# Optimization experiments

Measured on AMD Instinct MI355X. Metric: run time of the kernel, lower is better.

## Reference

```python
import jax, jax.numpy as jnp
import numpy as np

N_NODES = 50000
N_EDGES = 800000
D_IN = 256
D_OUT = 256
BN_EPS = 1e-5


def setup_inputs() -> dict:
    key = jax.random.key(0)
    k1, k2, k3 = jax.random.split(key, 3)
    x = jax.random.normal(k1, (N_NODES, D_IN), dtype=jnp.float32)
    edge_index = jax.random.randint(k2, (2, N_EDGES), 0, N_NODES, dtype=jnp.int64)
    # GCNConv linear weight [out, in] (glorot-ish scale), separate bias
    W = jax.random.normal(k3, (D_OUT, D_IN), dtype=jnp.float32) * (1.0 / np.sqrt(D_IN))
    bias = jnp.zeros((D_OUT,), dtype=jnp.float32)
    gamma = jnp.ones((D_OUT,), dtype=jnp.float32)
    beta = jnp.zeros((D_OUT,), dtype=jnp.float32)
    return {"x": x, "edge_index": edge_index, "W": W, "bias": bias, "gamma": gamma, "beta": beta}


def reference(x, edge_index, W, bias, gamma, beta):
    N = x.shape[0]
    self_loops = jnp.arange(N, dtype=edge_index.dtype)
    row = jnp.concatenate([edge_index[0], self_loops])  # source nodes
    col = jnp.concatenate([edge_index[1], self_loops])  # target nodes

    # linear transform first (PyG GCNConv order): [N, D_out]
    h = x @ W.T

    # symmetric degree normalization with self-loops
    deg = jax.ops.segment_sum(jnp.ones_like(col, dtype=h.dtype), col, num_segments=N)
    dinv = jnp.where(deg > 0, jax.lax.rsqrt(deg), 0.0)
    norm = dinv[row] * dinv[col]  # [E+N]

    # gather -> scale -> scatter-add
    msg = h[row] * norm[:, None]                         # [E+N, D_out]
    agg = jax.ops.segment_sum(msg, col, num_segments=N)  # [N, D_out]
    agg = agg + bias

    # BatchNorm (training mode: batch stats over nodes, biased var)
    mean = jnp.mean(agg, axis=0)
    var = jnp.mean((agg - mean) ** 2, axis=0)
    y = gamma * (agg - mean) * jax.lax.rsqrt(var + BN_EPS) + beta
    return jax.nn.relu(y)
```

## Files before the change

### kernel.cpp

```cpp
#include <hip/hip_runtime.h>
#include <cstdio>

#define NN 50000
#define NE 800000
#define DD 256
#define CAP 32
#define WS_NEED 113080000UL

__attribute__((constructor)) static void r25_on_load(void) {
    fprintf(stderr, "R25SO_LOADED\n");
    fflush(stderr);
}

__device__ float b2f(unsigned short u) {
    union { unsigned int i; float f; } c;
    c.i = ((unsigned int)u) << 16;
    return c.f;
}
__device__ float clampf(float v) { return fminf(fmaxf(v, -65504.f), 65504.f); }
__device__ float rdF(const void* p, long long idx, int ff) {
    if (ff) return clampf(b2f(((const unsigned short*)p)[idx]));
    return clampf(((const float*)p)[idx]);
}
__device__ unsigned short f2b_rne(float f) {
    union { float f; unsigned int u; } c;
    c.f = f;
    unsigned int r = (c.u + 0x7FFFu + ((c.u >> 16) & 1u)) >> 16;
    return (unsigned short)r;
}

typedef __attribute__((ext_vector_type(8))) short bf16x8;
typedef __attribute__((ext_vector_type(4))) float f32x4;
typedef __attribute__((ext_vector_type(4))) _Float16 f16x4;
typedef __attribute__((ext_vector_type(8))) _Float16 f16x8;

__device__ int detect_ff(const unsigned short* xr) {
    __shared__ int dacc;
    if (threadIdx.x == 0) dacc = 0;
    __syncthreads();
    int g = 0;
    for (int j = 0; j < 4; j++) {
        unsigned short u = xr[(threadIdx.x * 4 + j) * 2];
        int e = (u >> 7) & 0xFF;
        if (u == 0 || u == 0x8000 || (e >= 100 && e <= 140)) g++;
    }
    atomicAdd(&dacc, g);
    __syncthreads();
    return dacc >= 922;
}

__global__ void k_setup(int* cnt, int* misc, const unsigned short* xr,
                        const int* ei, int* flags, const void* W, const void* bias,
                        const void* gamma, const void* beta, unsigned short* Wb,
                        float* pf) {
    int b = blockIdx.x;
    int t = threadIdx.x;
    if (b < 196) {
        int i = b * 256 + t;
        if (i < NN) cnt[i] = 0;
        if (i < 16) misc[i] = 0;
        return;
    }
    if (b == 196) {
        __shared__ int acc2;
        if (t == 0) acc2 = 0;
        int ff = detect_ff(xr);
        if (ei[2 * t + 1] != 0) atomicAdd(&acc2, 1);
        __syncthreads();
        if (t == 0) {
            flags[0] = ff;
            flags[1] = (acc2 == 0) ? 1 : 0;
        }
        pf[t] = rdF(bias, t, ff);
        pf[DD + t] = rdF(gamma, t, ff);
        pf[2 * DD + t] = rdF(beta, t, ff);
        return;
    }
    int ff = detect_ff(xr);
    int i = (b - 197) * 256 + t;
    Wb[i] = f2b_rne(rdF(W, i, ff));
}

__global__ void k_fill1(const int* raw, const int* flags, int* cnt, int* csrc,
                        int* ovf, int* novf) {
    int e = blockIdx.x * 256 + threadIdx.x;
    if (e >= NE) return;
    int f = flags[1];
    int r = f ? raw[2 * e] : raw[e];
    int c = f ? raw[2 * (NE + e)] : raw[NE + e];
    if ((unsigned int)c < NN && (unsigned int)r < NN) {
        int slot = atomicAdd(&cnt[c], 1);
        if (slot < CAP) {
            csrc[c * CAP + slot] = r;
        } else {
            int o = atomicAdd(novf, 1);
            ovf[2 * o] = c;
            ovf[2 * o + 1] = r;
        }
    }
}

__global__ void k_dinv(const int* cnt, float* dinv) {
    int i = blockIdx.x * 256 + threadIdx.x;
    if (i < NN) dinv[i] = rsqrtf((float)(cnt[i] + 1));
}

#define WP 264
__global__ __launch_bounds__(1024) void k_gemm(const void* x, const int* flags,
                                               const unsigned short* Wb,
                                               const float* dinv, _Float16* h) {
    __shared__ unsigned short wlds[256 * WP];
    int t = threadIdx.x;

#pragma unroll
    for (int i = 0; i < 8; i++) {
        int c = t + i * 1024;
        int row = c >> 5;
        int off = (c & 31) * 8;
        bf16x8 v = *(const bf16x8*)(Wb + row * DD + off);
        *(bf16x8*)(&wlds[row * WP + off]) = v;
    }
    __syncthreads();

    int wave = t >> 6;
    int lane = t & 63;
    int rw = blockIdx.x * 16 + wave;
    if (rw >= 3125) return;
    int r0 = rw * 16;
    int l15 = lane & 15;
    int kq = lane >> 4;

    bf16x8 a[8];
    int ff = flags[0];
    if (ff) {
        const unsigned short* p =
            (const unsigned short*)x + (unsigned long long)(r0 + l15) * DD + kq * 8;
#pragma unroll
        for (int k = 0; k < 8; k++)
            a[k] = *(const bf16x8*)(p + k * 32);
    } else {
        const float* p = (const float*)x + (unsigned long long)(r0 + l15) * DD + kq * 8;
#pragma unroll
        for (int k = 0; k < 8; k++) {
#pragma unroll
            for (int j = 0; j < 8; j++)
                a[k][j] = (short)f2b_rne(p[k * 32 + j]);
        }
    }

    float dv[4];
#pragma unroll
    for (int j = 0; j < 4; j++) dv[j] = dinv[r0 + kq * 4 + j];

#pragma unroll
    for (int ct = 0; ct < 16; ct++) {
        f32x4 acc = {0.f, 0.f, 0.f, 0.f};
#pragma unroll
        for (int k = 0; k < 8; k++) {
            bf16x8 b = *(const bf16x8*)(&wlds[(ct * 16 + l15) * WP + kq * 8 + k * 32]);
            acc = __builtin_amdgcn_mfma_f32_16x16x32_bf16(a[k], b, acc, 0, 0, 0);
        }
        _Float16* op = h + (unsigned long long)(r0 + kq * 4) * DD + ct * 16 + l15;
#pragma unroll
        for (int j = 0; j < 4; j++)
            op[(unsigned long long)j * DD] = (_Float16)(acc[j] * dv[j]);
    }
}

__global__ __launch_bounds__(256) void g_agg(const _Float16* h, const float* dinv,
                                             const int* cnt, const int* csrc,
                                             const int* ovf, const int* novf,
                                             const float* pf, _Float16* agg) {
    int lane = threadIdx.x & 63;
    int n = blockIdx.x * 4 + (threadIdx.x >> 6);
    int f0 = lane * 4;
    int cn = __builtin_amdgcn_readfirstlane(cnt[n]);
    int m = (cn < CAP) ? cn : CAP;
    float dn = dinv[n];
    f16x4 hv = *(const f16x4*)(h + (unsigned long long)n * DD + f0);
    float a0 = (float)hv[0];
    float a1 = (float)hv[1];
    float a2 = (float)hv[2];
    float a3 = (float)hv[3];
    const int* ip = csrc + n * CAP;
    int k = 0;
    for (; k + 8 <= m; k += 8) {
        int i0 = ip[k + 0], i1 = ip[k + 1], i2 = ip[k + 2], i3 = ip[k + 3];
        int i4 = ip[k + 4], i5 = ip[k + 5], i6 = ip[k + 6], i7 = ip[k + 7];
        f16x4 v0 = *(const f16x4*)(h + (unsigned long long)i0 * DD + f0);
        f16x4 v1 = *(const f16x4*)(h + (unsigned long long)i1 * DD + f0);
        f16x4 v2 = *(const f16x4*)(h + (unsigned long long)i2 * DD + f0);
        f16x4 v3 = *(const f16x4*)(h + (unsigned long long)i3 * DD + f0);
        f16x4 v4 = *(const f16x4*)(h + (unsigned long long)i4 * DD + f0);
        f16x4 v5 = *(const f16x4*)(h + (unsigned long long)i5 * DD + f0);
        f16x4 v6 = *(const f16x4*)(h + (unsigned long long)i6 * DD + f0);
        f16x4 v7 = *(const f16x4*)(h + (unsigned long long)i7 * DD + f0);
        a0 += (((float)v0[0] + (float)v1[0]) + ((float)v2[0] + (float)v3[0])) +
              (((float)v4[0] + (float)v5[0]) + ((float)v6[0] + (float)v7[0]));
        a1 += (((float)v0[1] + (float)v1[1]) + ((float)v2[1] + (float)v3[1])) +
              (((float)v4[1] + (float)v5[1]) + ((float)v6[1] + (float)v7[1]));
        a2 += (((float)v0[2] + (float)v1[2]) + ((float)v2[2] + (float)v3[2])) +
              (((float)v4[2] + (float)v5[2]) + ((float)v6[2] + (float)v7[2]));
        a3 += (((float)v0[3] + (float)v1[3]) + ((float)v2[3] + (float)v3[3])) +
              (((float)v4[3] + (float)v5[3]) + ((float)v6[3] + (float)v7[3]));
    }
    for (; k + 4 <= m; k += 4) {
        int i0 = ip[k + 0], i1 = ip[k + 1], i2 = ip[k + 2], i3 = ip[k + 3];
        f16x4 v0 = *(const f16x4*)(h + (unsigned long long)i0 * DD + f0);
        f16x4 v1 = *(const f16x4*)(h + (unsigned long long)i1 * DD + f0);
        f16x4 v2 = *(const f16x4*)(h + (unsigned long long)i2 * DD + f0);
        f16x4 v3 = *(const f16x4*)(h + (unsigned long long)i3 * DD + f0);
        a0 += ((float)v0[0] + (float)v1[0]) + ((float)v2[0] + (float)v3[0]);
        a1 += ((float)v0[1] + (float)v1[1]) + ((float)v2[1] + (float)v3[1]);
        a2 += ((float)v0[2] + (float)v1[2]) + ((float)v2[2] + (float)v3[2]);
        a3 += ((float)v0[3] + (float)v1[3]) + ((float)v2[3] + (float)v3[3]);
    }
    for (; k < m; k++) {
        int i0 = ip[k];
        f16x4 v0 = *(const f16x4*)(h + (unsigned long long)i0 * DD + f0);
        a0 += (float)v0[0];
        a1 += (float)v0[1];
        a2 += (float)v0[2];
        a3 += (float)v0[3];
    }
    if (cn > CAP) {
        int no = __builtin_amdgcn_readfirstlane(*novf);
        for (int i = 0; i < no; i++) {
            if (ovf[2 * i] == n) {
                int r = ovf[2 * i + 1];
                f16x4 v0 = *(const f16x4*)(h + (unsigned long long)r * DD + f0);
                a0 += (float)v0[0];
                a1 += (float)v0[1];
                a2 += (float)v0[2];
                a3 += (float)v0[3];
            }
        }
    }
    f16x4 o;
    o[0] = (_Float16)(dn * a0 + pf[f0 + 0]);
    o[1] = (_Float16)(dn * a1 + pf[f0 + 1]);
    o[2] = (_Float16)(dn * a2 + pf[f0 + 2]);
    o[3] = (_Float16)(dn * a3 + pf[f0 + 3]);
    *(f16x4*)(agg + (unsigned long long)n * DD + f0) = o;
}

__global__ __launch_bounds__(256) void k_stats1(const _Float16* agg, float* pstat) {
    __shared__ float ls[2][DD];
    int t = threadIdx.x;
    int rg = t >> 5;
    int cg = t & 31;
    float s[8], s2[8];
#pragma unroll
    for (int j = 0; j < 8; j++) { s[j] = 0.f; s2[j] = 0.f; }
    int row0 = blockIdx.x * 64;
    int rend = row0 + 64;
    if (rend > NN) rend = NN;
    for (int r = row0 + rg; r < rend; r += 8) {
        f16x8 v = *(const f16x8*)(agg + (unsigned long long)r * DD + cg * 8);
#pragma unroll
        for (int j = 0; j < 8; j++) {
            float f = (float)v[j];
            s[j] += f;
            s2[j] += f * f;
        }
    }
    ls[0][t] = 0.f;
    ls[1][t] = 0.f;
    __syncthreads();
#pragma unroll
    for (int j = 0; j < 8; j++) {
        atomicAdd(&ls[0][cg * 8 + j], s[j]);
        atomicAdd(&ls[1][cg * 8 + j], s2[j]);
    }
    __syncthreads();
    float* pb = pstat + (unsigned long long)blockIdx.x * 512;
    pb[t] = ls[0][t];
    pb[256 + t] = ls[1][t];
}

__global__ __launch_bounds__(256) void k_stats2(const float* pstat, const float* pf,
                                                float* ss) {
    __shared__ float ls[16][16];
    int t = threadIdx.x;
    int r = t >> 4;
    int c = t & 15;
    int j = blockIdx.x;
    int slot = (c < 8) ? (j * 8 + c) : (256 + j * 8 + (c - 8));
    float acc = 0.f;
    for (int b = r; b < 782; b += 16)
        acc += pstat[(unsigned long long)b * 512 + slot];
    ls[r][c] = acc;
    __syncthreads();
    for (int step = 8; step >= 1; step >>= 1) {
        if (r < step) ls[r][c] += ls[r + step][c];
        __syncthreads();
    }
    if (t < 8) {
        int f = j * 8 + t;
        float sv = ls[0][t];
        float sv2 = ls[0][t + 8];
        float mean = sv * (1.0f / NN);
        float var = fmaxf(sv2 * (1.0f / NN) - mean * mean, 0.f);
        float sc = pf[DD + f] * rsqrtf(var + 1e-5f);
        ss[f] = sc;
        ss[DD + f] = pf[2 * DD + f] - mean * sc;
    }
}

__global__ void DenseGCNLayer_2937757631000_kernel(const _Float16* agg, const float* ss,
                                                   float* out) {
    int t = threadIdx.x;
    unsigned long long base =
        (unsigned long long)blockIdx.x * 2048 + (unsigned int)t * 8;
    int f = (int)(base & 255);
    f16x8 v = *(const f16x8*)(agg + base);
    f32x4 o0, o1;
#pragma unroll
    for (int j = 0; j < 4; j++)
        o0[j] = fmaxf(ss[f + j] * (float)v[j] + ss[DD + f + j], 0.f);
#pragma unroll
    for (int j = 0; j < 4; j++)
        o1[j] = fmaxf(ss[f + 4 + j] * (float)v[4 + j] + ss[DD + f + 4 + j], 0.f);
    *(f32x4*)(out + base) = o0;
    *(f32x4*)(out + base + 4) = o1;
}

extern "C" void kernel_launch(void* const* d_in, const int* in_sizes, int n_in,
                              void* d_out, int out_size, void* d_ws, size_t ws_size,
                              hipStream_t stream) {
    const void* x = d_in[0];
    const int* ei = (const int*)d_in[1];
    const void* W = d_in[2];
    const void* bias = d_in[3];
    const void* gamma = d_in[4];
    const void* beta = d_in[5];
    char* ws = (char*)d_ws;
    float* out = (float*)d_out;

    _Float16* h = (_Float16*)(ws + 0UL);
    _Float16* agg = (_Float16*)(ws + 51200000UL);
    int* ovf = (int*)(ws + 80000000UL);
    float* pstat = (float*)(ws + 102400000UL);
    int* csrc = (int*)(ws + 104800000UL);
    unsigned short* Wb = (unsigned short*)(ws + 112000000UL);
    int* cnt = (int*)(ws + 112262144UL);
    float* dinv = (float*)(ws + 112462336UL);
    int* misc = (int*)(ws + 113063936UL);
    float* pf = (float*)(ws + 113064960UL);
    float* ss = (float*)(ws + 113070080UL);
    int* flags = (int*)(ws + 113072128UL);

    if (ws_size < WS_NEED) {
        fprintf(stderr, "R25_WS_SMALL %zu\n", ws_size);
        fflush(stderr);
        return;
    }

    k_setup<<<453, 256, 0, stream>>>(cnt, misc, (const unsigned short*)x, ei,
                                     flags, W, bias, gamma, beta, Wb, pf);
    k_fill1<<<3125, 256, 0, stream>>>(ei, flags, cnt, csrc, ovf, &misc[0]);
    k_dinv<<<196, 256, 0, stream>>>(cnt, dinv);
    k_gemm<<<196, 1024, 0, stream>>>(x, flags, Wb, dinv, h);
    g_agg<<<12500, 256, 0, stream>>>(h, dinv, cnt, csrc, ovf, &misc[0], pf, agg);
    k_stats1<<<782, 256, 0, stream>>>(agg, pstat);
    k_stats2<<<32, 256, 0, stream>>>(pstat, pf, ss);
    DenseGCNLayer_2937757631000_kernel<<<6250, 256, 0, stream>>>(agg, ss, out);
}
```

Baseline: 288.1 us.

## Bucket edges by target range before CSR fill and inline degree rsqrt

Edge insertion is split into a partition pass that groups edges into eight target-node buckets using block-local counters, followed by a fill pass that processes each bucket with interleaved blocks, so that atomics and csrc writes land in a narrower address range. The separate dinv kernel is removed and rsqrt(cnt+1) is computed inline in the GEMM and aggregation kernels. This adds an extra pass over the edges plus an intermediate queue write and read, and it relies on misc[8..15] being zeroed by setup, which is not visible here.

```diff
diff --git a/kernel.cpp b/kernel.cpp
--- a/kernel.cpp
+++ b/kernel.cpp
@@ -5,10 +5,11 @@
 #define NE 800000
 #define DD 256
 #define CAP 32
+#define QCAP 200000
 #define WS_NEED 113080000UL
 
-__attribute__((constructor)) static void r25_on_load(void) {
-    fprintf(stderr, "R25SO_LOADED\n");
+__attribute__((constructor)) static void r26_on_load(void) {
+    fprintf(stderr, "R26SO_LOADED\n");
     fflush(stderr);
 }
 
@@ -81,34 +82,73 @@
     Wb[i] = f2b_rne(rdF(W, i, ff));
 }
 
-__global__ void k_fill1(const int* raw, const int* flags, int* cnt, int* csrc,
-                        int* ovf, int* novf) {
-    int e = blockIdx.x * 256 + threadIdx.x;
-    if (e >= NE) return;
-    int f = flags[1];
-    int r = f ? raw[2 * e] : raw[e];
-    int c = f ? raw[2 * (NE + e)] : raw[NE + e];
-    if ((unsigned int)c < NN && (unsigned int)r < NN) {
-        int slot = atomicAdd(&cnt[c], 1);
+__global__ __launch_bounds__(256) void k_parta(const int* raw, const int* flags,
+                                               int2* eq, int* qcnt, int* cnt,
+                                               int* csrc, int* ovf, int* novf) {
+    __shared__ int lcnt[8];
+    __shared__ int lbase[8];
+    int t = threadIdx.x;
+    if (t < 8) lcnt[t] = 0;
+    __syncthreads();
+    int e = blockIdx.x * 256 + t;
+    int valid = 0, r = 0, c = 0, b = 0, pos = 0;
+    if (e < NE) {
+        int f = flags[1];
+        r = f ? raw[2 * e] : raw[e];
+        c = f ? raw[2 * (NE + e)] : raw[NE + e];
+        if ((unsigned int)c < NN && (unsigned int)r < NN) {
+            valid = 1;
+            b = c / 6250;
+            pos = atomicAdd(&lcnt[b], 1);
+        }
+    }
+    __syncthreads();
+    if (t < 8) lbase[t] = atomicAdd(&qcnt[t], lcnt[t]);
+    __syncthreads();
+    if (valid) {
+        int idx = lbase[b] + pos;
+        if (idx < QCAP) {
+            int2 p;
+            p.x = c;
+            p.y = r;
+            eq[b * QCAP + idx] = p;
+        } else {
+            int slot = atomicAdd(&cnt[c], 1);
+            if (slot < CAP) {
+                csrc[c * CAP + slot] = r;
+            } else {
+                int o = atomicAdd(novf, 1);
+                ovf[2 * o] = c;
+                ovf[2 * o + 1] = r;
+            }
+        }
+    }
+}
+
+__global__ __launch_bounds__(256) void k_fillb(const int2* eq, const int* qcnt,
+                                               int* cnt, int* csrc, int* ovf,
+                                               int* novf) {
+    int k = blockIdx.x & 7;
+    int s = blockIdx.x >> 3;
+    int n = qcnt[k];
+    if (n > QCAP) n = QCAP;
+    for (int i = s * 256 + threadIdx.x; i < n; i += 391 * 256) {
+        int2 p = eq[k * QCAP + i];
+        int slot = atomicAdd(&cnt[p.x], 1);
         if (slot < CAP) {
-            csrc[c * CAP + slot] = r;
+            csrc[p.x * CAP + slot] = p.y;
         } else {
             int o = atomicAdd(novf, 1);
-            ovf[2 * o] = c;
-            ovf[2 * o + 1] = r;
-        }
-    }
-}
-
-__global__ void k_dinv(const int* cnt, float* dinv) {
-    int i = blockIdx.x * 256 + threadIdx.x;
-    if (i < NN) dinv[i] = rsqrtf((float)(cnt[i] + 1));
+            ovf[2 * o] = p.x;
+            ovf[2 * o + 1] = p.y;
+        }
+    }
 }
 
 #define WP 264
 __global__ __launch_bounds__(1024) void k_gemm(const void* x, const int* flags,
                                                const unsigned short* Wb,
-                                               const float* dinv, _Float16* h) {
+                                               const int* cnt, _Float16* h) {
     __shared__ unsigned short wlds[256 * WP];
     int t = threadIdx.x;
 
@@ -150,7 +190,8 @@
 
     float dv[4];
 #pragma unroll
-    for (int j = 0; j < 4; j++) dv[j] = dinv[r0 + kq * 4 + j];
+    for (int j = 0; j < 4; j++)
+        dv[j] = rsqrtf((float)(cnt[r0 + kq * 4 + j] + 1));
 
 #pragma unroll
     for (int ct = 0; ct < 16; ct++) {
@@ -167,16 +208,16 @@
     }
 }
 
-__global__ __launch_bounds__(256) void g_agg(const _Float16* h, const float* dinv,
-                                             const int* cnt, const int* csrc,
-                                             const int* ovf, const int* novf,
-                                             const float* pf, _Float16* agg) {
+__global__ __launch_bounds__(256) void g_agg(const _Float16* h, const int* cnt,
+                                             const int* csrc, const int* ovf,
+                                             const int* novf, const float* pf,
+                                             _Float16* agg) {
     int lane = threadIdx.x & 63;
     int n = blockIdx.x * 4 + (threadIdx.x >> 6);
     int f0 = lane * 4;
     int cn = __builtin_amdgcn_readfirstlane(cnt[n]);
     int m = (cn < CAP) ? cn : CAP;
-    float dn = dinv[n];
+    float dn = rsqrtf((float)(cn + 1));
     f16x4 hv = *(const f16x4*)(h + (unsigned long long)n * DD + f0);
     float a0 = (float)hv[0];
     float a1 = (float)hv[1];
@@ -338,30 +379,31 @@
     float* out = (float*)d_out;
 
     _Float16* h = (_Float16*)(ws + 0UL);
+    int2* eq = (int2*)(ws + 25600000UL);
     _Float16* agg = (_Float16*)(ws + 51200000UL);
     int* ovf = (int*)(ws + 80000000UL);
     float* pstat = (float*)(ws + 102400000UL);
     int* csrc = (int*)(ws + 104800000UL);
     unsigned short* Wb = (unsigned short*)(ws + 112000000UL);
     int* cnt = (int*)(ws + 112262144UL);
-    float* dinv = (float*)(ws + 112462336UL);
     int* misc = (int*)(ws + 113063936UL);
     float* pf = (float*)(ws + 113064960UL);
     float* ss = (float*)(ws + 113070080UL);
     int* flags = (int*)(ws + 113072128UL);
 
     if (ws_size < WS_NEED) {
-        fprintf(stderr, "R25_WS_SMALL %zu\n", ws_size);
+        fprintf(stderr, "R26_WS_SMALL %zu\n", ws_size);
         fflush(stderr);
         return;
     }
 
     k_setup<<<453, 256, 0, stream>>>(cnt, misc, (const unsigned short*)x, ei,
                                      flags, W, bias, gamma, beta, Wb, pf);
-    k_fill1<<<3125, 256, 0, stream>>>(ei, flags, cnt, csrc, ovf, &misc[0]);
-    k_dinv<<<196, 256, 0, stream>>>(cnt, dinv);
-    k_gemm<<<196, 1024, 0, stream>>>(x, flags, Wb, dinv, h);
-    g_agg<<<12500, 256, 0, stream>>>(h, dinv, cnt, csrc, ovf, &misc[0], pf, agg);
+    k_parta<<<3125, 256, 0, stream>>>(ei, flags, eq, &misc[8], cnt, csrc, ovf,
+                                      &misc[0]);
+    k_fillb<<<3128, 256, 0, stream>>>(eq, &misc[8], cnt, csrc, ovf, &misc[0]);
+    k_gemm<<<196, 1024, 0, stream>>>(x, flags, Wb, cnt, h);
+    g_agg<<<12500, 256, 0, stream>>>(h, cnt, csrc, ovf, &misc[0], pf, agg);
     k_stats1<<<782, 256, 0, stream>>>(agg, pstat);
     k_stats2<<<32, 256, 0, stream>>>(pstat, pf, ss);
     DenseGCNLayer_2937757631000_kernel<<<6250, 256, 0, stream>>>(agg, ss, out);
```

Measured after the change: 305.5 us. 1.06x slower.
